# Performance work log

Hardware: AMD Instinct MI355X
Metric: run time of the kernel (lower is better)

Reference implementation:

```python
import jax, jax.numpy as jnp
import numpy as np

D_MODEL = 1024
NUM_HEADS = 16
D_K = D_MODEL // NUM_HEADS
D_FF = 4096
THETA = 10000.0
EPS = 1e-5


def rmsnorm(x, w):
    ms = jnp.mean(jnp.square(x), axis=-1, keepdims=True)
    return x * jax.lax.rsqrt(ms + EPS) * w


def rope(x, pos):
    # x: [B, H, S, d_k]; pos: [S]
    half = x.shape[-1] // 2
    inv_freq = THETA ** (-jnp.arange(half, dtype=x.dtype) * 2.0 / x.shape[-1])  # [half]
    ang = pos.astype(x.dtype)[:, None] * inv_freq[None, :]  # [S, half]
    cos, sin = jnp.cos(ang), jnp.sin(ang)
    xe, xo = x[..., 0::2], x[..., 1::2]
    oe = xe * cos - xo * sin
    oo = xe * sin + xo * cos
    return jnp.stack([oe, oo], axis=-1).reshape(x.shape)


def setup_inputs() -> dict:
    key = jax.random.key(0)
    ks = jax.random.split(key, 10)
    std_d = 1.0 / np.sqrt(D_MODEL)
    std_f = 1.0 / np.sqrt(D_FF)
    B, S = 4, 2048
    return {
        "x": jax.random.normal(ks[0], (B, S, D_MODEL), dtype=jnp.float32),
        "token_positions": jnp.arange(S, dtype=jnp.int32),
        "q_proj": jax.random.normal(ks[1], (D_MODEL, D_MODEL), dtype=jnp.float32) * std_d,
        "k_proj": jax.random.normal(ks[2], (D_MODEL, D_MODEL), dtype=jnp.float32) * std_d,
        "v_proj": jax.random.normal(ks[3], (D_MODEL, D_MODEL), dtype=jnp.float32) * std_d,
        "o_proj": jax.random.normal(ks[4], (D_MODEL, D_MODEL), dtype=jnp.float32) * std_d,
        "w1": jax.random.normal(ks[5], (D_FF, D_MODEL), dtype=jnp.float32) * std_d,
        "w2": jax.random.normal(ks[6], (D_MODEL, D_FF), dtype=jnp.float32) * std_f,
        "w3": jax.random.normal(ks[7], (D_FF, D_MODEL), dtype=jnp.float32) * std_d,
        "ln1_w": jnp.ones((D_MODEL,), dtype=jnp.float32),
        "ln2_w": jnp.ones((D_MODEL,), dtype=jnp.float32),
    }


def reference(x, token_positions, q_proj, k_proj, v_proj, o_proj, w1, w2, w3, ln1_w, ln2_w):
    B, S, _ = x.shape
    x_ln = rmsnorm(x, ln1_w)
    q = x_ln @ q_proj.T
    k = x_ln @ k_proj.T
    v = x_ln @ v_proj.T
    # [B, S, D] -> [B, H, S, d_k]
    def split_heads(t):
        return t.reshape(B, S, NUM_HEADS, D_K).transpose(0, 2, 1, 3)
    q, k, v = split_heads(q), split_heads(k), split_heads(v)
    q = rope(q, token_positions)
    k = rope(k, token_positions)
    scores = jnp.einsum("bhqd,bhkd->bhqk", q, k) / jnp.sqrt(jnp.asarray(D_K, x.dtype))
    causal = jnp.tril(jnp.ones((S, S), dtype=bool))
    scores = jnp.where(causal, scores, -jnp.inf)
    attn = jax.nn.softmax(scores, axis=-1)
    out = jnp.einsum("bhqk,bhkd->bhqd", attn, v)
    out = out.transpose(0, 2, 1, 3).reshape(B, S, D_MODEL)
    x = x + out @ o_proj.T
    x_ln2 = rmsnorm(x, ln2_w)
    u = x_ln2 @ w1.T
    vff = x_ln2 @ w3.T
    ff = (u * jax.nn.sigmoid(u)) * vff
    return x + ff @ w2.T
```

## Files before the change

kernel.cpp:

```cpp
#include <hip/hip_runtime.h>
#include <hip/hip_bf16.h>


typedef unsigned short u16;
typedef __attribute__((ext_vector_type(8))) short short8;
typedef __attribute__((ext_vector_type(4))) float f32x4;
typedef __attribute__((ext_vector_type(16))) float f32x16;

#define MFMA16(a, b, c) __builtin_amdgcn_mfma_f32_16x16x32_bf16(a, b, c, 0, 0, 0)
#define MFMA32(a, b, c) __builtin_amdgcn_mfma_f32_32x32x16_bf16(a, b, c, 0, 0, 0)
#define VMC(N) asm volatile("s_waitcnt vmcnt(" #N ")" ::: "memory")

__device__ __forceinline__ u16 f2b(float f) {
  union { float f; unsigned u; } x; x.f = f;
  unsigned r = x.u + 0x7FFFu + ((x.u >> 16) & 1u);
  return (u16)(r >> 16);
}
__device__ __forceinline__ float b2f(u16 h) {
  union { unsigned u; float f; } x; x.u = ((unsigned)h) << 16;
  return x.f;
}
__device__ __forceinline__ unsigned pkbf(float a, float b) {
  __hip_bfloat162 h = __float22bfloat162_rn(make_float2(a, b));
  union { __hip_bfloat162 h; unsigned u; } cv; cv.h = h;
  return cv.u;
}
__device__ __forceinline__ void async16(const void* g, void* l) {
  __builtin_amdgcn_global_load_lds(
      (const __attribute__((address_space(1))) void*)g,
      (__attribute__((address_space(3))) void*)l, 16, 0, 0);
}

template <int MODE>
__global__ __launch_bounds__(256, 2) void gemm_bt(
    const u16* __restrict__ A, const u16* __restrict__ B,
    u16* __restrict__ Cb, float* __restrict__ Cf, const float* __restrict__ R,
    int M, int N, int K) {
  __shared__ __align__(16) u16 As[128 * 64];
  __shared__ __align__(16) u16 Bs[128 * 64];
  const int tid = threadIdx.x;
  const int l = tid & 63, w = tid >> 6;
  const int wr = w & 1, wc = w >> 1;
  const int lr = l & 31, lh = l >> 5;
  const size_t m0 = (size_t)blockIdx.y * 128, n0 = (size_t)blockIdx.x * 128;
  f32x16 acc[2][2] = {};
  for (int k0 = 0; k0 < K; k0 += 64) {
#pragma unroll
    for (int t = 0; t < 4; ++t) {
      int c = t * 256 + tid;
      int r = c >> 3;
      int gc = ((c & 7) ^ (r & 7)) << 3;
      async16(A + (m0 + r) * (size_t)K + k0 + gc, &As[c * 8]);
    }
#pragma unroll
    for (int t = 0; t < 4; ++t) {
      int c = t * 256 + tid;
      int r = c >> 3;
      int gc = ((c & 7) ^ (r & 7)) << 3;
      async16(B + (n0 + r) * (size_t)K + k0 + gc, &Bs[c * 8]);
    }
    __syncthreads();
#pragma unroll
    for (int c = 0; c < 4; ++c) {
      const int c8 = c * 2 + lh;
      short8 af[2], bfr[2];
#pragma unroll
      for (int mi = 0; mi < 2; ++mi) {
        int r = wr * 64 + mi * 32 + lr;
        af[mi] = *(const short8*)&As[r * 64 + ((c8 ^ (r & 7)) << 3)];
      }
#pragma unroll
      for (int ni = 0; ni < 2; ++ni) {
        int r = wc * 64 + ni * 32 + lr;
        bfr[ni] = *(const short8*)&Bs[r * 64 + ((c8 ^ (r & 7)) << 3)];
      }
#pragma unroll
      for (int mi = 0; mi < 2; ++mi)
#pragma unroll
        for (int ni = 0; ni < 2; ++ni)
          acc[mi][ni] = MFMA32(af[mi], bfr[ni], acc[mi][ni]);
    }
    __syncthreads();
  }
#pragma unroll
  for (int mi = 0; mi < 2; ++mi)
#pragma unroll
    for (int ni = 0; ni < 2; ++ni) {
      size_t n = n0 + wc * 64 + ni * 32 + lr;
#pragma unroll
      for (int reg = 0; reg < 16; ++reg) {
        size_t m = m0 + wr * 64 + mi * 32 + (reg & 3) + 8 * (reg >> 2) + 4 * lh;
        float v = acc[mi][ni][reg];
        if (MODE == 0)
          Cb[m * (size_t)N + n] = f2b(v);
        else
          Cf[m * (size_t)N + n] = v + R[m * (size_t)N + n];
      }
    }
}

__global__ __launch_bounds__(256, 2) void ffn_gemm(
    const u16* __restrict__ A, const u16* __restrict__ B1,
    const u16* __restrict__ B3, u16* __restrict__ Hout, int M, int N, int K) {
  __shared__ __align__(16) u16 As[128 * 64];
  __shared__ __align__(16) u16 B1s[128 * 64];
  __shared__ __align__(16) u16 B3s[128 * 64];
  const int tid = threadIdx.x;
  const int l = tid & 63, w = tid >> 6;
  const int wr = w & 1, wc = w >> 1;
  const int lr = l & 31, lh = l >> 5;
  const size_t m0 = (size_t)blockIdx.y * 128, n0 = (size_t)blockIdx.x * 128;
  f32x16 a1[2][2] = {}, a3[2][2] = {};
  for (int k0 = 0; k0 < K; k0 += 64) {
#pragma unroll
    for (int t = 0; t < 4; ++t) {
      int c = t * 256 + tid;
      int r = c >> 3;
      int gc = ((c & 7) ^ (r & 7)) << 3;
      async16(A + (m0 + r) * (size_t)K + k0 + gc, &As[c * 8]);
      async16(B1 + (n0 + r) * (size_t)K + k0 + gc, &B1s[c * 8]);
      async16(B3 + (n0 + r) * (size_t)K + k0 + gc, &B3s[c * 8]);
    }
    __syncthreads();
#pragma unroll
    for (int c = 0; c < 4; ++c) {
      const int c8 = c * 2 + lh;
      short8 af[2], b1f[2], b3f[2];
#pragma unroll
      for (int mi = 0; mi < 2; ++mi) {
        int r = wr * 64 + mi * 32 + lr;
        af[mi] = *(const short8*)&As[r * 64 + ((c8 ^ (r & 7)) << 3)];
      }
#pragma unroll
      for (int ni = 0; ni < 2; ++ni) {
        int r = wc * 64 + ni * 32 + lr;
        b1f[ni] = *(const short8*)&B1s[r * 64 + ((c8 ^ (r & 7)) << 3)];
        b3f[ni] = *(const short8*)&B3s[r * 64 + ((c8 ^ (r & 7)) << 3)];
      }
#pragma unroll
      for (int mi = 0; mi < 2; ++mi)
#pragma unroll
        for (int ni = 0; ni < 2; ++ni) {
          a1[mi][ni] = MFMA32(af[mi], b1f[ni], a1[mi][ni]);
          a3[mi][ni] = MFMA32(af[mi], b3f[ni], a3[mi][ni]);
        }
    }
    __syncthreads();
  }
#pragma unroll
  for (int mi = 0; mi < 2; ++mi)
#pragma unroll
    for (int ni = 0; ni < 2; ++ni) {
      size_t n = n0 + wc * 64 + ni * 32 + lr;
#pragma unroll
      for (int reg = 0; reg < 16; ++reg) {
        size_t m = m0 + wr * 64 + mi * 32 + (reg & 3) + 8 * (reg >> 2) + 4 * lh;
        float u = a1[mi][ni][reg];
        float g = u / (1.0f + __expf(-u));
        Hout[m * (size_t)N + n] = f2b(g * a3[mi][ni][reg]);
      }
    }
}

__global__ __launch_bounds__(256, 2) void attn_k(
    const u16* __restrict__ qh, const u16* __restrict__ kh,
    const u16* __restrict__ vt, u16* __restrict__ aout) {
  __shared__ __align__(16) u16 Ks[128 * 64];
  __shared__ __align__(16) u16 Vs[64 * 128];
  __shared__ __align__(16) u16 Ps[128 * 136];
  const int tid = threadIdx.x;
  const int l = tid & 63, w = tid >> 6;
  const int q = l & 15, lq = l >> 4;
  const int bh = blockIdx.y;
  const size_t base = (size_t)bh * (2048 * 64);
  const int b = bh >> 4, h = bh & 15;

#define STAGE_K(kvt)                                                          \
  { _Pragma("unroll") for (int t = 0; t < 4; ++t) {                           \
      int p = t * 256 + tid;                                                  \
      int r = p >> 3, cs = p & 7;                                             \
      async16(kh + base + (size_t)((kvt) * 128 + r) * 64 + ((cs ^ (r & 7)) << 3), \
              &Ks[p * 8]); } }
#define STAGE_V(kvt)                                                          \
  { _Pragma("unroll") for (int t = 0; t < 4; ++t) {                           \
      int p = t * 256 + tid;                                                  \
      int r = p >> 4, cs = p & 15;                                            \
      async16(vt + base + (size_t)r * 2048 + (kvt) * 128 + ((cs ^ (r & 15)) << 3), \
              &Vs[p * 8]); } }
#define BARRIER                                                               \
  __builtin_amdgcn_sched_barrier(0);                                          \
  __builtin_amdgcn_s_barrier();                                               \
  __builtin_amdgcn_sched_barrier(0)

#pragma unroll 1
  for (int pass = 0; pass < 2; ++pass) {
    const int qt = pass ? (int)blockIdx.x : 15 - (int)blockIdx.x;
    const int q0 = qt << 7;
    const int nt = qt + 1;
    const int qcol[2] = {q0 + w * 16 + q, q0 + 64 + w * 16 + q};
    short8 bq[2][2];
#pragma unroll
    for (int sub = 0; sub < 2; ++sub)
#pragma unroll
      for (int kk = 0; kk < 2; ++kk)
        bq[sub][kk] = *(const short8*)(qh + base + (size_t)qcol[sub] * 64 + kk * 32 + lq * 8);

    f32x4 o[2][4] = {};
    float mI[2] = {-1e30f, -1e30f}, lI[2] = {0.0f, 0.0f};
    u16* pr0 = &Ps[(w * 16 + q) * 136];
    u16* pr1 = &Ps[(64 + w * 16 + q) * 136];

    BARRIER;
    STAGE_K(0);
    STAGE_V(0);

#pragma unroll 1
    for (int it = 0; it < nt; ++it) {
      if (it == 0) { VMC(4); } else { VMC(0); }
      BARRIER;
      if (it) STAGE_V(it);

      f32x4 s[2][8] = {};
#pragma unroll
      for (int kk = 0; kk < 2; ++kk) {
#pragma unroll
        for (int mt = 0; mt < 8; ++mt) {
          int row = mt * 16 + q;
          short8 ak = *(const short8*)&Ks[row * 64 + (((kk * 4 + lq) ^ (q & 7)) << 3)];
          s[0][mt] = MFMA16(ak, bq[0][kk], s[0][mt]);
          s[1][mt] = MFMA16(ak, bq[1][kk], s[1][mt]);
        }
      }
      BARRIER;
      if (it + 1 < nt) STAGE_K(it + 1);

      const bool last = (it == nt - 1);
      if (last) {
        const int kv0 = it << 7;
#pragma unroll
        for (int sub = 0; sub < 2; ++sub)
#pragma unroll
          for (int mt = 0; mt < 8; ++mt)
#pragma unroll
            for (int r = 0; r < 4; ++r)
              if (kv0 + mt * 16 + lq * 4 + r > qcol[sub]) s[sub][mt][r] = -1e30f;
      }
#pragma unroll
      for (int sub = 0; sub < 2; ++sub) {
        float mx = -1e30f;
#pragma unroll
        for (int mt = 0; mt < 8; ++mt)
#pragma unroll
          for (int r = 0; r < 4; ++r) mx = fmaxf(mx, s[sub][mt][r]);
        mx = fmaxf(mx, __shfl_xor(mx, 16, 64));
        mx = fmaxf(mx, __shfl_xor(mx, 32, 64));
        const float mn = fmaxf(mI[sub], mx);
        const float al = exp2f(mI[sub] - mn);
        mI[sub] = mn;
        float rs = 0.0f;
#pragma unroll
        for (int mt = 0; mt < 8; ++mt)
#pragma unroll
          for (int r = 0; r < 4; ++r) {
            float p = exp2f(s[sub][mt][r] - mn);
            s[sub][mt][r] = p;
            rs += p;
          }
        rs += __shfl_xor(rs, 16, 64);
        rs += __shfl_xor(rs, 32, 64);
        lI[sub] = lI[sub] * al + rs;
#pragma unroll
        for (int mt = 0; mt < 4; ++mt)
#pragma unroll
          for (int r = 0; r < 4; ++r) o[sub][mt][r] *= al;
        u16* pr = sub ? pr1 : pr0;
#pragma unroll
        for (int mt = 0; mt < 8; ++mt) {
          uint2 pd;
          pd.x = pkbf(s[sub][mt][0], s[sub][mt][1]);
          pd.y = pkbf(s[sub][mt][2], s[sub][mt][3]);
          *(uint2*)&pr[mt * 16 + lq * 4] = pd;
        }
      }
      if (it + 1 < nt) { VMC(4); } else { VMC(0); }
      BARRIER;
#pragma unroll
      for (int kk = 0; kk < 4; ++kk) {
        short8 bp0 = *(const short8*)&pr0[kk * 32 + lq * 8];
        short8 bp1 = *(const short8*)&pr1[kk * 32 + lq * 8];
#pragma unroll
        for (int mt = 0; mt < 4; ++mt) {
          int row = mt * 16 + q;
          short8 av = *(const short8*)&Vs[row * 128 + (((kk * 4 + lq) ^ (row & 15)) << 3)];
          o[0][mt] = MFMA16(av, bp0, o[0][mt]);
          o[1][mt] = MFMA16(av, bp1, o[1][mt]);
        }
      }
    }
#pragma unroll
    for (int sub = 0; sub < 2; ++sub) {
      const float inv = 1.0f / lI[sub];
#pragma unroll
      for (int mt = 0; mt < 4; ++mt) {
        uint2 pd;
        pd.x = pkbf(o[sub][mt][0] * inv, o[sub][mt][1] * inv);
        pd.y = pkbf(o[sub][mt][2] * inv, o[sub][mt][3] * inv);
        *(uint2*)&aout[((size_t)(b * 2048 + qcol[sub])) * 1024 + h * 64 + mt * 16 + lq * 4] = pd;
      }
    }
  }
#undef STAGE_K
#undef STAGE_V
#undef BARRIER
}

__global__ __launch_bounds__(256) void rmsnorm_k(
    const float* __restrict__ x, const float* __restrict__ w, u16* __restrict__ out) {
  const int row = blockIdx.x;
  const int tid = threadIdx.x;
  const float4 v = ((const float4*)(x + (size_t)row * 1024))[tid];
  float ss = v.x * v.x + v.y * v.y + v.z * v.z + v.w * v.w;
#pragma unroll
  for (int d = 1; d < 64; d <<= 1) ss += __shfl_xor(ss, d, 64);
  __shared__ float red[4];
  if ((tid & 63) == 0) red[tid >> 6] = ss;
  __syncthreads();
  const float sc = rsqrtf((red[0] + red[1] + red[2] + red[3]) * (1.0f / 1024.0f) + 1e-5f);
  const float4 wv = ((const float4*)w)[tid];
  u16* o = out + (size_t)row * 1024 + tid * 4;
  o[0] = f2b(v.x * sc * wv.x);
  o[1] = f2b(v.y * sc * wv.y);
  o[2] = f2b(v.z * sc * wv.z);
  o[3] = f2b(v.w * sc * wv.w);
}

__global__ __launch_bounds__(256) void rope_k(
    const u16* __restrict__ qkv, u16* __restrict__ qh, u16* __restrict__ kh,
    const int* __restrict__ pos) {
  int idx = blockIdx.x * 256 + threadIdx.x;
  int grp = idx & 255;
  int row = idx >> 8;
  int which = grp >> 7;
  int p = grp & 127;
  int s = row & 2047, b = row >> 11;
  int h = p >> 3, gi = p & 7;
  const u16* src = qkv + (size_t)row * 3072 + which * 1024 + h * 64 + gi * 8;
  uint4 in = *(const uint4*)src;
  const u16* e = (const u16*)&in;
  const float fp = (float)pos[s];
  const float scale = which ? 1.0f : 0.18033688011112042f;
  uint4 outv;
  unsigned* ov = (unsigned*)&outv;
#pragma unroll
  for (int j = 0; j < 4; ++j) {
    int i = gi * 4 + j;
    float xe = b2f(e[2 * j]), xo = b2f(e[2 * j + 1]);
    float inv = exp2f(-(float)(2 * i) * (13.287712379549449f / 64.0f));
    float ang = fp * inv;
    float sn, cs;
    __sincosf(ang, &sn, &cs);
    ov[j] = pkbf((xe * cs - xo * sn) * scale, (xe * sn + xo * cs) * scale);
  }
  u16* dst = (which ? kh : qh) + (((size_t)(b * 16 + h)) * 2048 + s) * 64 + gi * 8;
  *(uint4*)dst = outv;
}

__global__ __launch_bounds__(256) void transv_k(
    const u16* __restrict__ qkv, u16* __restrict__ vt) {
  __shared__ u16 t[64][65];
  const int bh = blockIdx.y, s0 = blockIdx.x * 64;
  const int b = bh >> 4, h = bh & 15;
  const int tid = threadIdx.x;
#pragma unroll
  for (int i = 0; i < 16; ++i) {
    int e = i * 256 + tid;
    int sl = e >> 6, d = e & 63;
    t[sl][d] = qkv[((size_t)(b * 2048 + s0 + sl)) * 3072 + 2048 + h * 64 + d];
  }
  __syncthreads();
#pragma unroll
  for (int i = 0; i < 16; ++i) {
    int e = i * 256 + tid;
    int d = e >> 6, sl = e & 63;
    vt[((size_t)(bh * 64 + d)) * 2048 + s0 + sl] = t[sl][d];
  }
}

__global__ __launch_bounds__(256) void cvt_all(
    const float* __restrict__ qp, const float* __restrict__ kp,
    const float* __restrict__ vp, const float* __restrict__ op,
    const float* __restrict__ w1, const float* __restrict__ w3,
    const float* __restrict__ w2,
    u16* __restrict__ WQKV, u16* __restrict__ WO,
    u16* __restrict__ W1, u16* __restrict__ W3, u16* __restrict__ W2) {
  int i = blockIdx.x * 256 + threadIdx.x;
  const float* src;
  u16* dst;
  int off;
  if (i < 1048576) {
    int seg = i >> 18, within = i & 262143;
    src = (seg == 0) ? qp : (seg == 1) ? kp : (seg == 2) ? vp : op;
    dst = (seg == 3) ? WO : WQKV + (size_t)seg * 1048576;
    off = within;
  } else {
    int j = i - 1048576;
    int seg = j >> 20;
    off = j & 1048575;
    src = (seg == 0) ? w1 : (seg == 1) ? w3 : w2;
    dst = (seg == 0) ? W1 : (seg == 1) ? W3 : W2;
  }
  float4 v = ((const float4*)src)[off];
  u16* o = dst + (size_t)off * 4;
  o[0] = f2b(v.x); o[1] = f2b(v.y); o[2] = f2b(v.z); o[3] = f2b(v.w);
}

extern "C" void kernel_launch(void* const* d_in, const int* in_sizes, int n_in,
                              void* d_out, int out_size, void* d_ws, size_t ws_size,
                              hipStream_t stream) {
  const float* x   = (const float*)d_in[0];
  const int*   pos = (const int*)d_in[1];
  const float* qp  = (const float*)d_in[2];
  const float* kp  = (const float*)d_in[3];
  const float* vp  = (const float*)d_in[4];
  const float* op  = (const float*)d_in[5];
  const float* w1  = (const float*)d_in[6];
  const float* w2  = (const float*)d_in[7];
  const float* w3  = (const float*)d_in[8];
  const float* ln1 = (const float*)d_in[9];
  const float* ln2 = (const float*)d_in[10];
  float* out = (float*)d_out;
  char* ws = (char*)d_ws;
  const size_t MB = 1024 * 1024;

  u16* WQKV = (u16*)(ws + 0 * MB);
  u16* WO   = (u16*)(ws + 6 * MB);
  u16* W1   = (u16*)(ws + 8 * MB);
  u16* W3   = (u16*)(ws + 16 * MB);
  u16* W2   = (u16*)(ws + 24 * MB);
  u16* XLN  = (u16*)(ws + 32 * MB);
  u16* QKV  = (u16*)(ws + 48 * MB);
  u16* QH   = (u16*)(ws + 96 * MB);
  u16* KH   = (u16*)(ws + 112 * MB);
  u16* VT   = (u16*)(ws + 128 * MB);
  u16* ATT  = (u16*)(ws + 48 * MB);
  u16* XLN2 = (u16*)(ws + 64 * MB);
  u16* Hbuf = (u16*)(ws + 80 * MB);
  (void)in_sizes; (void)n_in; (void)out_size; (void)ws_size;

  cvt_all<<<16384, 256, 0, stream>>>(qp, kp, vp, op, w1, w3, w2,
                                     WQKV, WO, W1, W3, W2);
  rmsnorm_k<<<8192, 256, 0, stream>>>(x, ln1, XLN);
  gemm_bt<0><<<dim3(24, 64), 256, 0, stream>>>(XLN, WQKV, QKV, nullptr, nullptr, 8192, 3072, 1024);
  rope_k<<<8192, 256, 0, stream>>>(QKV, QH, KH, pos);
  transv_k<<<dim3(32, 64), 256, 0, stream>>>(QKV, VT);
  attn_k<<<dim3(8, 64), 256, 0, stream>>>(QH, KH, VT, ATT);
  gemm_bt<1><<<dim3(8, 64), 256, 0, stream>>>(ATT, WO, nullptr, out, x, 8192, 1024, 1024);
  rmsnorm_k<<<8192, 256, 0, stream>>>(out, ln2, XLN2);
  ffn_gemm<<<dim3(32, 64), 256, 0, stream>>>(XLN2, W1, W3, Hbuf, 8192, 4096, 1024);
  gemm_bt<1><<<dim3(8, 64), 256, 0, stream>>>(Hbuf, W2, nullptr, out, out, 8192, 1024, 4096);
}
```

Baseline: 576.2 us.

## Rewrite FFN gate/up GEMM as 8-wave double-buffered pipelined kernel

Replaces the fused W1/W3 SwiGLU GEMM with a 512-thread kernel that uses a 256x128 tile, double-buffered LDS and staggered async prefetch of A and B tiles. Compute phases are interleaved with loads, and s_setprio is raised around the MFMA blocks. The goal is to hide global-load latency and increase reuse of the B tiles across a taller M tile. It also vectorises the bf16 stores in rmsnorm and in the weight conversion kernel. The cost is much more LDS per block (about 128KB), which may limit occupancy, plus many barriers.

```diff
diff --git a/kernel.cpp b/kernel.cpp
--- a/kernel.cpp
+++ b/kernel.cpp
@@ -99,65 +99,110 @@
     }
 }
 
-__global__ __launch_bounds__(256, 2) void ffn_gemm(
+__global__ __launch_bounds__(512, 2) void ffn8p(
     const u16* __restrict__ A, const u16* __restrict__ B1,
-    const u16* __restrict__ B3, u16* __restrict__ Hout, int M, int N, int K) {
-  __shared__ __align__(16) u16 As[128 * 64];
-  __shared__ __align__(16) u16 B1s[128 * 64];
-  __shared__ __align__(16) u16 B3s[128 * 64];
+    const u16* __restrict__ B3, u16* __restrict__ Hout,
+    int M, int N, int K) {
+  __shared__ __align__(16) u16 As[2][2][128 * 64];
+  __shared__ __align__(16) u16 B1s[2][128 * 64];
+  __shared__ __align__(16) u16 B3s[2][128 * 64];
   const int tid = threadIdx.x;
   const int l = tid & 63, w = tid >> 6;
-  const int wr = w & 1, wc = w >> 1;
+  const int wm = w >> 2, wn = w & 3;
   const int lr = l & 31, lh = l >> 5;
-  const size_t m0 = (size_t)blockIdx.y * 128, n0 = (size_t)blockIdx.x * 128;
-  f32x16 a1[2][2] = {}, a3[2][2] = {};
-  for (int k0 = 0; k0 < K; k0 += 64) {
-#pragma unroll
-    for (int t = 0; t < 4; ++t) {
-      int c = t * 256 + tid;
-      int r = c >> 3;
-      int gc = ((c & 7) ^ (r & 7)) << 3;
-      async16(A + (m0 + r) * (size_t)K + k0 + gc, &As[c * 8]);
-      async16(B1 + (n0 + r) * (size_t)K + k0 + gc, &B1s[c * 8]);
-      async16(B3 + (n0 + r) * (size_t)K + k0 + gc, &B3s[c * 8]);
-    }
-    __syncthreads();
-#pragma unroll
-    for (int c = 0; c < 4; ++c) {
-      const int c8 = c * 2 + lh;
-      short8 af[2], b1f[2], b3f[2];
-#pragma unroll
-      for (int mi = 0; mi < 2; ++mi) {
-        int r = wr * 64 + mi * 32 + lr;
-        af[mi] = *(const short8*)&As[r * 64 + ((c8 ^ (r & 7)) << 3)];
-      }
-#pragma unroll
-      for (int ni = 0; ni < 2; ++ni) {
-        int r = wc * 64 + ni * 32 + lr;
-        b1f[ni] = *(const short8*)&B1s[r * 64 + ((c8 ^ (r & 7)) << 3)];
-        b3f[ni] = *(const short8*)&B3s[r * 64 + ((c8 ^ (r & 7)) << 3)];
-      }
-#pragma unroll
-      for (int mi = 0; mi < 2; ++mi)
-#pragma unroll
-        for (int ni = 0; ni < 2; ++ni) {
-          a1[mi][ni] = MFMA32(af[mi], b1f[ni], a1[mi][ni]);
-          a3[mi][ni] = MFMA32(af[mi], b3f[ni], a3[mi][ni]);
-        }
-    }
-    __syncthreads();
-  }
-#pragma unroll
-  for (int mi = 0; mi < 2; ++mi)
-#pragma unroll
-    for (int ni = 0; ni < 2; ++ni) {
-      size_t n = n0 + wc * 64 + ni * 32 + lr;
+  const size_t m0 = (size_t)blockIdx.y * 256, n0 = (size_t)blockIdx.x * 128;
+  f32x16 aU[2][2] = {}, aV[2][2] = {};
+
+#define STG_A(dd, hh, kt)                                                    \
+  { const size_t kofs = (size_t)(kt) * 64;                                   \
+    _Pragma("unroll") for (int j = 0; j < 2; ++j) {                          \
+      int p = j * 512 + tid;                                                 \
+      int r = p >> 3, c8 = p & 7;                                            \
+      async16(A + (m0 + (hh) * 128 + r) * (size_t)K + kofs                   \
+                  + (((c8) ^ (r & 7)) << 3),                                 \
+              &As[dd][hh][p * 8]); } }
+#define STG_B(dd, kt, Bp, Bls)                                               \
+  { const size_t kofs = (size_t)(kt) * 64;                                   \
+    _Pragma("unroll") for (int j = 0; j < 2; ++j) {                          \
+      int p = j * 512 + tid;                                                 \
+      int r = p >> 3, c8 = p & 7;                                            \
+      async16(Bp + (n0 + r) * (size_t)K + kofs + (((c8) ^ (r & 7)) << 3),    \
+              &Bls[dd][p * 8]); } }
+#define RD_A(QM)                                                             \
+  _Pragma("unroll") for (int c = 0; c < 4; ++c) {                            \
+    const int c8 = c * 2 + lh;                                               \
+    _Pragma("unroll") for (int mi = 0; mi < 2; ++mi) {                       \
+      int rr = (QM) * 64 + mi * 32 + lr;                                     \
+      af[mi][c] = *(const short8*)&As[d][wm][rr * 64 + (((c8) ^ (rr & 7)) << 3)]; \
+    } }
+#define RD_B(dst, Bls)                                                       \
+  _Pragma("unroll") for (int c = 0; c < 4; ++c) {                            \
+    const int c8 = c * 2 + lh;                                               \
+    const int rb = wn * 32 + lr;                                             \
+    dst[c] = *(const short8*)&Bls[d][rb * 64 + (((c8) ^ (rb & 7)) << 3)];    \
+  }
+#define MMX(accq, bfx)                                                       \
+  __builtin_amdgcn_s_setprio(1);                                             \
+  _Pragma("unroll") for (int c = 0; c < 4; ++c)                              \
+    _Pragma("unroll") for (int mi = 0; mi < 2; ++mi)                         \
+      accq[mi] = MFMA32(af[mi][c], bfx[c], accq[mi]);                        \
+  __builtin_amdgcn_s_setprio(0);
+#define SB0 __builtin_amdgcn_sched_barrier(0)
+#define BARX { SB0; __builtin_amdgcn_s_barrier(); SB0; }
+#define LGKM0 { asm volatile("s_waitcnt lgkmcnt(0)" ::: "memory"); SB0; }
+
+  const int NT = K >> 6;
+  STG_A(0, 0, 0); STG_A(0, 1, 0);
+  STG_B(0, 0, B1, B1s); STG_B(0, 0, B3, B3s);
+  STG_B(1, 1, B1, B1s); STG_B(1, 1, B3, B3s);
+  VMC(4);
+  SB0;
+  __builtin_amdgcn_s_barrier();
+
+  short8 af[2][4], b1f[4], b3f[4];
+
+  for (int t = 0; t < NT; ++t) {
+    const int d = t & 1;
+    RD_A(0); RD_B(b1f, B1s);
+    if (t + 1 < NT) STG_A(d ^ 1, 0, t + 1);
+    BARX; LGKM0;
+    MMX(aU[0], b1f);
+    BARX;
+    RD_B(b3f, B3s);
+    if (t + 1 < NT) STG_A(d ^ 1, 1, t + 1);
+    BARX; LGKM0;
+    MMX(aV[0], b3f);
+    BARX;
+    RD_A(1);
+    if (t + 2 < NT) STG_B(d, t + 2, B1, B1s);
+    BARX; LGKM0;
+    MMX(aU[1], b1f);
+    BARX;
+    if (t + 2 < NT) STG_B(d, t + 2, B3, B3s);
+    BARX; LGKM0;
+    MMX(aV[1], b3f);
+    if (t + 2 < NT) { VMC(4); }
+    else if (t + 1 < NT) { VMC(0); }
+    SB0;
+    BARX;
+  }
+#undef STG_A
+#undef STG_B
+#undef RD_A
+#undef RD_B
+#undef MMX
+
+#pragma unroll
+  for (int qm = 0; qm < 2; ++qm)
+#pragma unroll
+    for (int mi = 0; mi < 2; ++mi) {
+      size_t n = n0 + wn * 32 + lr;
 #pragma unroll
       for (int reg = 0; reg < 16; ++reg) {
-        size_t m = m0 + wr * 64 + mi * 32 + (reg & 3) + 8 * (reg >> 2) + 4 * lh;
-        float u = a1[mi][ni][reg];
+        size_t m = m0 + wm * 128 + qm * 64 + mi * 32 + (reg & 3) + 8 * (reg >> 2) + 4 * lh;
+        float u = aU[qm][mi][reg];
         float g = u / (1.0f + __expf(-u));
-        Hout[m * (size_t)N + n] = f2b(g * a3[mi][ni][reg]);
+        Hout[m * (size_t)N + n] = f2b(g * aV[qm][mi][reg]);
       }
     }
 }
@@ -327,11 +372,10 @@
   __syncthreads();
   const float sc = rsqrtf((red[0] + red[1] + red[2] + red[3]) * (1.0f / 1024.0f) + 1e-5f);
   const float4 wv = ((const float4*)w)[tid];
-  u16* o = out + (size_t)row * 1024 + tid * 4;
-  o[0] = f2b(v.x * sc * wv.x);
-  o[1] = f2b(v.y * sc * wv.y);
-  o[2] = f2b(v.z * sc * wv.z);
-  o[3] = f2b(v.w * sc * wv.w);
+  uint2 pv;
+  pv.x = pkbf(v.x * sc * wv.x, v.y * sc * wv.y);
+  pv.y = pkbf(v.z * sc * wv.z, v.w * sc * wv.w);
+  *(uint2*)(out + (size_t)row * 1024 + tid * 4) = pv;
 }
 
 __global__ __launch_bounds__(256) void rope_k(
@@ -410,8 +454,10 @@
     dst = (seg == 0) ? W1 : (seg == 1) ? W3 : W2;
   }
   float4 v = ((const float4*)src)[off];
-  u16* o = dst + (size_t)off * 4;
-  o[0] = f2b(v.x); o[1] = f2b(v.y); o[2] = f2b(v.z); o[3] = f2b(v.w);
+  uint2 pv;
+  pv.x = pkbf(v.x, v.y);
+  pv.y = pkbf(v.z, v.w);
+  *(uint2*)(dst + (size_t)off * 4) = pv;
 }
 
 extern "C" void kernel_launch(void* const* d_in, const int* in_sizes, int n_in,
@@ -456,6 +502,6 @@
   attn_k<<<dim3(8, 64), 256, 0, stream>>>(QH, KH, VT, ATT);
   gemm_bt<1><<<dim3(8, 64), 256, 0, stream>>>(ATT, WO, nullptr, out, x, 8192, 1024, 1024);
   rmsnorm_k<<<8192, 256, 0, stream>>>(out, ln2, XLN2);
-  ffn_gemm<<<dim3(32, 64), 256, 0, stream>>>(XLN2, W1, W3, Hbuf, 8192, 4096, 1024);
+  ffn8p<<<dim3(32, 32), 512, 0, stream>>>(XLN2, W1, W3, Hbuf, 8192, 4096, 1024);
   gemm_bt<1><<<dim3(8, 64), 256, 0, stream>>>(Hbuf, W2, nullptr, out, out, 8192, 1024, 4096);
 }
```

New measurement: 574.0 us. No clear change (-0.4%).
